# Optimization experiments

Hardware: AMD Instinct MI355X
Metric: run time of the kernel (lower is better)

## Reference

```python
import jax, jax.numpy as jnp
import numpy as np
import math

EMB = 2048
HEADS = 16
HEAD_DIM = EMB // HEADS  # 128
SCALE = math.sqrt(HEAD_DIM)


def srms_norm(x, eps_min=1e-12):
    # Scaled RMS norm over last dim, computed in float32.
    d = x.shape[-1]
    xf = x.astype(jnp.float32)
    norm = jnp.linalg.norm(xf * (1.0 / math.sqrt(d)), axis=-1, keepdims=True)
    norm = jnp.maximum(norm, eps_min)
    return (xf / norm).astype(x.dtype)


def setup_inputs() -> dict:
    key = jax.random.key(0)
    ks = jax.random.split(key, 6)
    x = jax.random.normal(ks[0], (4, 4096, EMB), dtype=jnp.float32)
    # xavier-normal std for square D x D: sqrt(2/(D+D)) = 1/sqrt(D); gain=1 (lth=None)
    std = 1.0 / math.sqrt(EMB)
    Wq = jax.random.normal(ks[1], (EMB, EMB), dtype=jnp.float32) * std
    Wk = jax.random.normal(ks[2], (EMB, EMB), dtype=jnp.float32) * std
    Wv = jax.random.normal(ks[3], (EMB, EMB), dtype=jnp.float32) * std
    Wu = jax.random.normal(ks[4], (EMB, EMB), dtype=jnp.float32) * std
    Wo = jax.random.normal(ks[5], (EMB, EMB), dtype=jnp.float32) * std
    return {"x": x, "Wq": Wq, "Wk": Wk, "Wv": Wv, "Wu": Wu, "Wo": Wo}


def reference(x, Wq, Wk, Wv, Wu, Wo):
    B, L, D = x.shape
    H, dh = HEADS, HEAD_DIM
    # projections (weights stored as [in, out])
    q = (x @ Wq).reshape(B, L, H, dh).transpose(0, 2, 1, 3)  # [B,H,L,dh]
    k = (x @ Wk).reshape(B, L, H, dh).transpose(0, 2, 1, 3)
    v = (x @ Wv).reshape(B, L, H, dh).transpose(0, 2, 1, 3)
    u = (x @ Wu).reshape(B, L, H, dh).transpose(0, 2, 1, 3)
    q = jax.nn.relu(q) / SCALE
    k = jax.nn.relu(k) / SCALE
    u = jax.nn.silu(u)
    # linear retention: kv state [B,H,dh,dh], then q @ kv
    kv = jnp.einsum('bhlk,bhlv->bhkv', k, v)
    out = jnp.einsum('bhlk,bhkv->bhlv', q, kv)
    out = srms_norm(out) * u
    out = out.transpose(0, 2, 1, 3).reshape(B, L, D)
    return out @ Wo
```

## Files before the change

### kernel.cpp

```cpp
#include <hip/hip_runtime.h>
#include <hip/hip_bf16.h>
#include <cstdint>


typedef __attribute__((ext_vector_type(8))) short short8;
typedef __attribute__((ext_vector_type(4))) float f32x4;

#define DEVI static __device__ __forceinline__

DEVI float bf2f(unsigned short u) {
    union { unsigned int i; float f; } w; w.i = ((unsigned int)u) << 16; return w.f;
}
DEVI unsigned short f2bf(float f) {
    union { float f; unsigned int i; } w; w.f = f;
    return (unsigned short)((w.i + 0x7fffu + ((w.i >> 16) & 1u)) >> 16);
}

#define GLDS16(gp, lp) __builtin_amdgcn_global_load_lds( \
    (const __attribute__((address_space(1))) void*)(gp), \
    (__attribute__((address_space(3))) void*)(lp), 16, 0, 0)

__global__ void probe_dtype(const unsigned short* __restrict__ x, int* flag) {
    __shared__ int cnt;
    if (threadIdx.x == 0) cnt = 0;
    __syncthreads();
    int c = 0;
    for (int i = threadIdx.x; i < 4096; i += 256) {
        float a = fabsf(bf2f(x[i]));
        if (!(a <= 1e4f) || (a != 0.0f && a < 1e-4f)) ++c;
    }
    atomicAdd(&cnt, c);
    __syncthreads();
    if (threadIdx.x == 0) *flag = (cnt < 512) ? 1 : 0;
}

__global__ void wconvert(const void* __restrict__ Wq, const void* __restrict__ Wk,
                         const void* __restrict__ Wv, const void* __restrict__ Wu,
                         const void* __restrict__ Wo,
                         unsigned short* __restrict__ wt4,
                         unsigned short* __restrict__ wot,
                         const int* __restrict__ flag) {
    const int z = blockIdx.z;
    const void* W = (z == 0) ? Wq : (z == 1) ? Wk : (z == 2) ? Wv : (z == 3) ? Wu : Wo;
    const bool isbf = (*flag != 0);
    __shared__ float tile[32][33];
    const int j0 = blockIdx.x * 32, i0 = blockIdx.y * 32;
    const int tx = threadIdx.x, ty = threadIdx.y;
#pragma unroll
    for (int r = 0; r < 4; ++r) {
        const int i = i0 + ty * 4 + r;
        float v;
        if (isbf) v = bf2f(((const unsigned short*)W)[i * 2048 + j0 + tx]);
        else      v = ((const float*)W)[i * 2048 + j0 + tx];
        tile[ty * 4 + r][tx] = v;
    }
    __syncthreads();
#pragma unroll
    for (int r = 0; r < 4; ++r) {
        const int j = j0 + ty * 4 + r;
        const unsigned short bv = f2bf(tile[tx][ty * 4 + r]);
        if (z < 4) wt4[(long)(z * 2048 + j) * 2048 + i0 + tx] = bv;
        else       wot[(long)j * 2048 + i0 + tx] = bv;
    }
}

__global__ void xconvert(const void* __restrict__ X, unsigned short* __restrict__ xb,
                         const int* __restrict__ flag) {
    const bool isbf = (*flag != 0);
    const long i = (long)blockIdx.x * 256 + threadIdx.x;
    if (isbf) {
        ((uint4*)xb)[i] = ((const uint4*)X)[i];
    } else {
        const float4 f0 = ((const float4*)X)[2 * i];
        const float4 f1 = ((const float4*)X)[2 * i + 1];
        union { unsigned short us[8]; uint4 v; } o;
        o.us[0] = f2bf(f0.x); o.us[1] = f2bf(f0.y); o.us[2] = f2bf(f0.z); o.us[3] = f2bf(f0.w);
        o.us[4] = f2bf(f1.x); o.us[5] = f2bf(f1.y); o.us[6] = f2bf(f1.z); o.us[7] = f2bf(f1.w);
        ((uint4*)xb)[i] = o.v;
    }
}

__global__ void gemm_qkvu(const unsigned short* __restrict__ Xb,
                          const unsigned short* __restrict__ Wt4,
                          unsigned short* __restrict__ Qb, unsigned short* __restrict__ Kb,
                          unsigned short* __restrict__ Vb, unsigned short* __restrict__ Ub) {
    __shared__ unsigned short As[128 * 32];
    __shared__ unsigned short Bs[128 * 32];
    const int orig = blockIdx.x;
    const int swz = (orig & 7) * 1024 + (orig >> 3);
    const int m0 = (swz & 127) * 128;
    const int nt = swz >> 7;
    const int j0 = nt * 128;
    const int tid = threadIdx.x;
    const int wave = tid >> 6, lane = tid & 63;
    const int wr = wave >> 1, wc = wave & 1;
    const int srow = tid >> 2;
    const int scol = (tid & 3) * 8;
    f32x4 acc[4][4] = {};

    for (int kt = 0; kt < 64; ++kt) {
        __syncthreads();
        const int kb = kt * 32;
#pragma unroll
        for (int i = 0; i < 2; ++i) {
            GLDS16(Xb  + (long)(m0 + i * 64 + srow) * 2048 + kb + scol, As + i * 2048 + wave * 512);
            GLDS16(Wt4 + (long)(j0 + i * 64 + srow) * 2048 + kb + scol, Bs + i * 2048 + wave * 512);
        }
        __syncthreads();
        short8 a[4], b[4];
#pragma unroll
        for (int fm = 0; fm < 4; ++fm)
            a[fm] = *(const short8*)(As + (wr * 64 + fm * 16 + (lane & 15)) * 32 + (lane >> 4) * 8);
#pragma unroll
        for (int fn = 0; fn < 4; ++fn)
            b[fn] = *(const short8*)(Bs + (wc * 64 + fn * 16 + (lane & 15)) * 32 + (lane >> 4) * 8);
#pragma unroll
        for (int fm = 0; fm < 4; ++fm)
#pragma unroll
            for (int fn = 0; fn < 4; ++fn)
                acc[fm][fn] = __builtin_amdgcn_mfma_f32_16x16x32_bf16(a[fm], b[fn], acc[fm][fn], 0, 0, 0);
    }

    const int seg = nt >> 4;
    unsigned short* outp = (seg == 0) ? Qb : (seg == 1) ? Kb : (seg == 2) ? Vb : Ub;
    const int cl0 = (nt & 15) * 128 + wc * 64;
#pragma unroll
    for (int fm = 0; fm < 4; ++fm) {
#pragma unroll
        for (int fn = 0; fn < 4; ++fn) {
            const int col = cl0 + fn * 16 + (lane & 15);
#pragma unroll
            for (int r = 0; r < 4; ++r) {
                const long row = m0 + wr * 64 + fm * 16 + ((lane >> 4) << 2) + r;
                float v = acc[fm][fn][r];
                if (seg <= 1)      v = fmaxf(v, 0.0f) * 0.08838834764831845f;
                else if (seg == 3) v = v / (1.0f + __expf(-v));
                outp[row * 2048 + col] = f2bf(v);
            }
        }
    }
}

__global__ void kv_accum(const unsigned short* __restrict__ Kb,
                         const unsigned short* __restrict__ Vb,
                         float* __restrict__ KVpart) {
    __shared__ unsigned short Kt[128 * 64];
    __shared__ unsigned short Vt[128 * 64];
    const int bh = blockIdx.x;
    const int chunk = blockIdx.y;
    const int b = bh >> 4, h = bh & 15;
    const int t = threadIdx.x, wave = t >> 6, lane = t & 63;
    const int wr = wave >> 1, wc = wave & 1;
    const int l0 = (t & 15) * 4;
    const int dkg = t >> 4;
    const long gbase = ((long)b * 4096 + chunk * 1024) * 2048 + h * 128;
    f32x4 acc[4][4] = {};

    for (int tile = 0; tile < 16; ++tile) {
        __syncthreads();
        short8 kr[4], vr[4];
#pragma unroll
        for (int li = 0; li < 4; ++li) {
            const long go = gbase + (long)(tile * 64 + l0 + li) * 2048 + dkg * 8;
            kr[li] = *(const short8*)(Kb + go);
            vr[li] = *(const short8*)(Vb + go);
        }
#pragma unroll
        for (int i = 0; i < 8; ++i) {
            const int row = dkg * 8 + i;
            const int lin = row * 128 + l0 * 2;
            const int off = (lin ^ ((row & 7) << 4)) >> 1;
            union { unsigned short us[4]; unsigned long long u; } pk, pv;
#pragma unroll
            for (int li = 0; li < 4; ++li) { pk.us[li] = (unsigned short)kr[li][i]; pv.us[li] = (unsigned short)vr[li][i]; }
            *(unsigned long long*)(Kt + off) = pk.u;
            *(unsigned long long*)(Vt + off) = pv.u;
        }
        __syncthreads();
#pragma unroll
        for (int ks = 0; ks < 2; ++ks) {
            const int kof = ks * 64 + (lane >> 4) * 16;
            short8 a[4], bfr[4];
#pragma unroll
            for (int f = 0; f < 4; ++f) {
                const int ra = wr * 64 + f * 16 + (lane & 15);
                const int rb = wc * 64 + f * 16 + (lane & 15);
                a[f]   = *(const short8*)(Vt + (((ra * 128 + kof) ^ ((ra & 7) << 4)) >> 1));
                bfr[f] = *(const short8*)(Kt + (((rb * 128 + kof) ^ ((rb & 7) << 4)) >> 1));
            }
#pragma unroll
            for (int fm = 0; fm < 4; ++fm)
#pragma unroll
                for (int fn = 0; fn < 4; ++fn)
                    acc[fm][fn] = __builtin_amdgcn_mfma_f32_16x16x32_bf16(a[fm], bfr[fn], acc[fm][fn], 0, 0, 0);
        }
    }
    float* dst = KVpart + ((long)chunk * 64 + bh) * 16384;
#pragma unroll
    for (int fm = 0; fm < 4; ++fm)
#pragma unroll
        for (int fn = 0; fn < 4; ++fn)
#pragma unroll
            for (int r = 0; r < 4; ++r) {
                const int dv = wr * 64 + fm * 16 + ((lane >> 4) << 2) + r;
                const int dk = wc * 64 + fn * 16 + (lane & 15);
                dst[dv * 128 + dk] = acc[fm][fn][r];
            }
}

__global__ void kv_finalize(const float* __restrict__ KVpart,
                            unsigned short* __restrict__ KVhi,
                            unsigned short* __restrict__ KVlo) {
    const long base = ((long)blockIdx.x * 256 + threadIdx.x) * 4;
    float4 s0 = *(const float4*)(KVpart + base);
    const float4 s1 = *(const float4*)(KVpart + 1048576 + base);
    const float4 s2 = *(const float4*)(KVpart + 2097152 + base);
    const float4 s3 = *(const float4*)(KVpart + 3145728 + base);
    float s[4] = { s0.x + s1.x + s2.x + s3.x, s0.y + s1.y + s2.y + s3.y,
                   s0.z + s1.z + s2.z + s3.z, s0.w + s1.w + s2.w + s3.w };
    union { unsigned short us[4]; unsigned long long u; } hi, lo;
#pragma unroll
    for (int j = 0; j < 4; ++j) {
        hi.us[j] = f2bf(s[j]);
        lo.us[j] = f2bf(s[j] - bf2f(hi.us[j]));
    }
    *(unsigned long long*)(KVhi + base) = hi.u;
    *(unsigned long long*)(KVlo + base) = lo.u;
}

__global__ void o_norm(const unsigned short* __restrict__ Qb,
                       const unsigned short* __restrict__ Ub,
                       const unsigned short* __restrict__ KVhi,
                       const unsigned short* __restrict__ KVlo,
                       unsigned short* __restrict__ Ob) {
    __shared__ unsigned short Qs[128 * 128];
    const int tid = threadIdx.x, wave = tid >> 6, lane = tid & 63;
    const int tile = blockIdx.x;
    const int bh = blockIdx.y;
    const int b = bh >> 4, h = bh & 15;
    const long n0 = (long)b * 4096 + tile * 128;

    const int qrow = tid >> 4;
    const int qcol = (tid & 15) * 8;
#pragma unroll
    for (int i = 0; i < 8; ++i)
        GLDS16(Qb + (n0 + i * 16 + qrow) * 2048 + h * 128 + qcol, Qs + i * 2048 + wave * 512);
    __syncthreads();

    const unsigned short* KH = KVhi + (long)bh * 16384;
    const unsigned short* KL = KVlo + (long)bh * 16384;
    f32x4 acc[2][8] = {};
#pragma unroll
    for (int kk = 0; kk < 4; ++kk) {
        const short8 a0 = *(const short8*)(Qs + (wave * 32 + (lane & 15)) * 128 + kk * 32 + (lane >> 4) * 8);
        const short8 a1 = *(const short8*)(Qs + (wave * 32 + 16 + (lane & 15)) * 128 + kk * 32 + (lane >> 4) * 8);
#pragma unroll
        for (int fn = 0; fn < 8; ++fn) {
            const int bo = (fn * 16 + (lane & 15)) * 128 + kk * 32 + (lane >> 4) * 8;
            const short8 bhi = *(const short8*)(KH + bo);
            const short8 blo = *(const short8*)(KL + bo);
            acc[0][fn] = __builtin_amdgcn_mfma_f32_16x16x32_bf16(a0, bhi, acc[0][fn], 0, 0, 0);
            acc[0][fn] = __builtin_amdgcn_mfma_f32_16x16x32_bf16(a0, blo, acc[0][fn], 0, 0, 0);
            acc[1][fn] = __builtin_amdgcn_mfma_f32_16x16x32_bf16(a1, bhi, acc[1][fn], 0, 0, 0);
            acc[1][fn] = __builtin_amdgcn_mfma_f32_16x16x32_bf16(a1, blo, acc[1][fn], 0, 0, 0);
        }
    }

#pragma unroll
    for (int fm = 0; fm < 2; ++fm) {
#pragma unroll
        for (int r = 0; r < 4; ++r) {
            float ssq = 0.0f;
#pragma unroll
            for (int fn = 0; fn < 8; ++fn) { const float v = acc[fm][fn][r]; ssq += v * v; }
            ssq += __shfl_xor(ssq, 1);
            ssq += __shfl_xor(ssq, 2);
            ssq += __shfl_xor(ssq, 4);
            ssq += __shfl_xor(ssq, 8);
            const float nrm = fmaxf(sqrtf(ssq) * 0.08838834764831845f, 1e-12f);
            const float scl = 1.0f / nrm;
            const long row = n0 + wave * 32 + fm * 16 + ((lane >> 4) << 2) + r;
#pragma unroll
            for (int fn = 0; fn < 8; ++fn) {
                const int col = fn * 16 + (lane & 15);
                const float uv = bf2f(Ub[row * 2048 + h * 128 + col]);
                Ob[row * 2048 + h * 128 + col] = f2bf(acc[fm][fn][r] * scl * uv);
            }
        }
    }
}

__global__ void gemm_out(const unsigned short* __restrict__ Obuf,
                         const unsigned short* __restrict__ Wot,
                         void* __restrict__ out, const int* __restrict__ flag) {
    __shared__ unsigned short As[128 * 32];
    __shared__ unsigned short Bs[128 * 32];
    const int orig = blockIdx.x;
    const int swz = (orig & 7) * 256 + (orig >> 3);
    const int m0 = (swz & 127) * 128;
    const int j0 = (swz >> 7) * 128;
    const int tid = threadIdx.x;
    const int wave = tid >> 6, lane = tid & 63;
    const int wr = wave >> 1, wc = wave & 1;
    const int srow = tid >> 2;
    const int scol = (tid & 3) * 8;
    f32x4 acc[4][4] = {};

    for (int kt = 0; kt < 64; ++kt) {
        __syncthreads();
        const int kb = kt * 32;
#pragma unroll
        for (int i = 0; i < 2; ++i) {
            GLDS16(Obuf + (long)(m0 + i * 64 + srow) * 2048 + kb + scol, As + i * 2048 + wave * 512);
            GLDS16(Wot  + (long)(j0 + i * 64 + srow) * 2048 + kb + scol, Bs + i * 2048 + wave * 512);
        }
        __syncthreads();
        short8 a[4], b[4];
#pragma unroll
        for (int fm = 0; fm < 4; ++fm)
            a[fm] = *(const short8*)(As + (wr * 64 + fm * 16 + (lane & 15)) * 32 + (lane >> 4) * 8);
#pragma unroll
        for (int fn = 0; fn < 4; ++fn)
            b[fn] = *(const short8*)(Bs + (wc * 64 + fn * 16 + (lane & 15)) * 32 + (lane >> 4) * 8);
#pragma unroll
        for (int fm = 0; fm < 4; ++fm)
#pragma unroll
            for (int fn = 0; fn < 4; ++fn)
                acc[fm][fn] = __builtin_amdgcn_mfma_f32_16x16x32_bf16(a[fm], b[fn], acc[fm][fn], 0, 0, 0);
    }

    const bool isbf = (*flag != 0);
#pragma unroll
    for (int fm = 0; fm < 4; ++fm) {
#pragma unroll
        for (int fn = 0; fn < 4; ++fn) {
            const int col = j0 + wc * 64 + fn * 16 + (lane & 15);
#pragma unroll
            for (int r = 0; r < 4; ++r) {
                const long row = m0 + wr * 64 + fm * 16 + ((lane >> 4) << 2) + r;
                const float v = acc[fm][fn][r];
                if (isbf) ((unsigned short*)out)[row * 2048 + col] = f2bf(v);
                else      ((float*)out)[row * 2048 + col] = v;
            }
        }
    }
}

extern "C" void kernel_launch(void* const* d_in, const int* in_sizes, int n_in,
                              void* d_out, int out_size, void* d_ws, size_t ws_size,
                              hipStream_t stream) {
    (void)in_sizes; (void)n_in; (void)out_size; (void)ws_size;
    char* ws = (char*)d_ws;
    unsigned short* Xb  = (unsigned short*)(ws + 0);
    unsigned short* Wt4 = (unsigned short*)(ws + 67108864);
    unsigned short* Wot = (unsigned short*)(ws + 100663296);
    unsigned short* Qb  = (unsigned short*)(ws + 109051904);
    unsigned short* Kb  = (unsigned short*)(ws + 176160768);
    unsigned short* Vb  = (unsigned short*)(ws + 243269632);
    unsigned short* Ub  = (unsigned short*)(ws + 310378496);
    int*            flag= (int*)(ws + 381681664);
    float*          KVpart = (float*)Wt4;
    unsigned short* KVhi   = (unsigned short*)(ws + 67108864 + 16777216);
    unsigned short* KVlo   = (unsigned short*)(ws + 67108864 + 18874368);
    unsigned short* Ob     = Xb;

    probe_dtype<<<1, 256, 0, stream>>>((const unsigned short*)d_in[0], flag);
    wconvert<<<dim3(64, 64, 5), dim3(32, 8), 0, stream>>>(d_in[1], d_in[2], d_in[3],
                                                          d_in[4], d_in[5], Wt4, Wot, flag);
    xconvert<<<16384, 256, 0, stream>>>(d_in[0], Xb, flag);
    gemm_qkvu<<<8192, 256, 0, stream>>>(Xb, Wt4, Qb, Kb, Vb, Ub);
    kv_accum<<<dim3(64, 4), 256, 0, stream>>>(Kb, Vb, KVpart);
    kv_finalize<<<1024, 256, 0, stream>>>(KVpart, KVhi, KVlo);
    o_norm<<<dim3(32, 64), 256, 0, stream>>>(Qb, Ub, KVhi, KVlo, Ob);
    gemm_out<<<2048, 256, 0, stream>>>(Ob, Wot, d_out, flag);
}
```

Measured before the change: 1.109 ms.

## Rewrite projection GEMMs with 256x256 tiles, 4-stage LDS pipeline and swizzle

Both the QKVU and output GEMMs now share a core that uses 256x256 block tiles with 8 waves and a 4-deep ring of LDS buffers. Global-to-LDS loads are issued three stages ahead, with vmcnt waits in place of full syncthreads, and reads use an XOR-swizzled LDS layout to avoid bank conflicts. The core also raises wave priority around the MFMA block. The aim is more reuse per tile and memory latency hidden behind MFMA work, at the cost of 128KB of LDS per block, higher register pressure, and fewer blocks in flight.

```diff
diff --git a/kernel.cpp b/kernel.cpp
--- a/kernel.cpp
+++ b/kernel.cpp
@@ -80,62 +80,126 @@
     }
 }
 
-__global__ void gemm_qkvu(const unsigned short* __restrict__ Xb,
-                          const unsigned short* __restrict__ Wt4,
-                          unsigned short* __restrict__ Qb, unsigned short* __restrict__ Kb,
-                          unsigned short* __restrict__ Vb, unsigned short* __restrict__ Ub) {
-    __shared__ unsigned short As[128 * 32];
-    __shared__ unsigned short Bs[128 * 32];
+DEVI void gemm_core(const unsigned short* __restrict__ Ag,
+                    const unsigned short* __restrict__ Bg,
+                    unsigned short* As, unsigned short* Bs,
+                    f32x4 acc[8][4], const int tid) {
+    const int wave = tid >> 6, lane = tid & 63;
+    const int wr = wave >> 2, wc = wave & 3;
+    const int srow = tid >> 2;
+    const int lsl = (tid & 3) ^ ((srow >> 1) & 3);
+    const unsigned short* ga0 = Ag + (long)srow * 2048 + lsl * 8;
+    const unsigned short* ga1 = ga0 + 128 * 2048;
+    const unsigned short* gb0 = Bg + (long)srow * 2048 + lsl * 8;
+    const unsigned short* gb1 = gb0 + 128 * 2048;
+    const int ldsb = wave * 512;
+
+    const int psl = ((lane >> 4) ^ (((lane & 15) >> 1) & 3)) * 8;
+    const int abase = (wr * 128 + (lane & 15)) * 32 + psl;
+    const int bbase = (wc * 64 + (lane & 15)) * 32 + psl;
+
+#define ISSUE(tt) do { \
+    const int _b = (tt) & 3; const int _ko = (tt) * 32; \
+    GLDS16(ga0 + _ko, As + _b * 8192 + ldsb); \
+    GLDS16(ga1 + _ko, As + _b * 8192 + 4096 + ldsb); \
+    GLDS16(gb0 + _ko, Bs + _b * 8192 + ldsb); \
+    GLDS16(gb1 + _ko, Bs + _b * 8192 + 4096 + ldsb); \
+} while (0)
+
+    ISSUE(0); ISSUE(1); ISSUE(2);
+    for (int t = 0; t < 64; ++t) {
+        asm volatile("s_waitcnt vmcnt(8)" ::: "memory");
+        asm volatile("s_barrier" ::: "memory");
+        int tt = t + 3; if (tt >= 64) tt -= 64;
+        ISSUE(tt);
+        const unsigned short* a_ = As + (t & 3) * 8192;
+        const unsigned short* b_ = Bs + (t & 3) * 8192;
+        short8 af[8], bf[4];
+#pragma unroll
+        for (int fm = 0; fm < 8; ++fm) af[fm] = *(const short8*)(a_ + abase + fm * 512);
+#pragma unroll
+        for (int fn = 0; fn < 4; ++fn) bf[fn] = *(const short8*)(b_ + bbase + fn * 512);
+        __builtin_amdgcn_s_setprio(1);
+#pragma unroll
+        for (int fm = 0; fm < 8; ++fm)
+#pragma unroll
+            for (int fn = 0; fn < 4; ++fn)
+                acc[fm][fn] = __builtin_amdgcn_mfma_f32_16x16x32_bf16(af[fm], bf[fn], acc[fm][fn], 0, 0, 0);
+        __builtin_amdgcn_s_setprio(0);
+        asm volatile("s_barrier" ::: "memory");
+    }
+    asm volatile("s_waitcnt vmcnt(0)" ::: "memory");
+#undef ISSUE
+}
+
+__global__ __launch_bounds__(512, 2)
+void gemm_qkvu(const unsigned short* __restrict__ Xb,
+               const unsigned short* __restrict__ Wt4,
+               unsigned short* __restrict__ Qb, unsigned short* __restrict__ Kb,
+               unsigned short* __restrict__ Vb, unsigned short* __restrict__ Ub) {
+    __shared__ unsigned short As[4 * 8192];
+    __shared__ unsigned short Bs[4 * 8192];
     const int orig = blockIdx.x;
-    const int swz = (orig & 7) * 1024 + (orig >> 3);
-    const int m0 = (swz & 127) * 128;
-    const int nt = swz >> 7;
-    const int j0 = nt * 128;
+    const int flat = (orig & 7) * 256 + (orig >> 3);
+    const int mt = flat & 63, nt = flat >> 6;
+    const long m0 = (long)mt * 256;
     const int tid = threadIdx.x;
+    f32x4 acc[8][4] = {};
+
+    gemm_core(Xb + m0 * 2048, Wt4 + (long)nt * 256 * 2048, As, Bs, acc, tid);
+
     const int wave = tid >> 6, lane = tid & 63;
-    const int wr = wave >> 1, wc = wave & 1;
-    const int srow = tid >> 2;
-    const int scol = (tid & 3) * 8;
-    f32x4 acc[4][4] = {};
-
-    for (int kt = 0; kt < 64; ++kt) {
-        __syncthreads();
-        const int kb = kt * 32;
-#pragma unroll
-        for (int i = 0; i < 2; ++i) {
-            GLDS16(Xb  + (long)(m0 + i * 64 + srow) * 2048 + kb + scol, As + i * 2048 + wave * 512);
-            GLDS16(Wt4 + (long)(j0 + i * 64 + srow) * 2048 + kb + scol, Bs + i * 2048 + wave * 512);
-        }
-        __syncthreads();
-        short8 a[4], b[4];
-#pragma unroll
-        for (int fm = 0; fm < 4; ++fm)
-            a[fm] = *(const short8*)(As + (wr * 64 + fm * 16 + (lane & 15)) * 32 + (lane >> 4) * 8);
-#pragma unroll
-        for (int fn = 0; fn < 4; ++fn)
-            b[fn] = *(const short8*)(Bs + (wc * 64 + fn * 16 + (lane & 15)) * 32 + (lane >> 4) * 8);
-#pragma unroll
-        for (int fm = 0; fm < 4; ++fm)
-#pragma unroll
-            for (int fn = 0; fn < 4; ++fn)
-                acc[fm][fn] = __builtin_amdgcn_mfma_f32_16x16x32_bf16(a[fm], b[fn], acc[fm][fn], 0, 0, 0);
-    }
-
-    const int seg = nt >> 4;
+    const int wr = wave >> 2, wc = wave & 3;
+    const int seg = nt >> 3;
     unsigned short* outp = (seg == 0) ? Qb : (seg == 1) ? Kb : (seg == 2) ? Vb : Ub;
-    const int cl0 = (nt & 15) * 128 + wc * 64;
-#pragma unroll
-    for (int fm = 0; fm < 4; ++fm) {
+    const int cl0 = (nt & 7) * 256 + wc * 64;
+#pragma unroll
+    for (int fm = 0; fm < 8; ++fm) {
 #pragma unroll
         for (int fn = 0; fn < 4; ++fn) {
             const int col = cl0 + fn * 16 + (lane & 15);
 #pragma unroll
             for (int r = 0; r < 4; ++r) {
-                const long row = m0 + wr * 64 + fm * 16 + ((lane >> 4) << 2) + r;
+                const long row = m0 + wr * 128 + fm * 16 + ((lane >> 4) << 2) + r;
                 float v = acc[fm][fn][r];
                 if (seg <= 1)      v = fmaxf(v, 0.0f) * 0.08838834764831845f;
                 else if (seg == 3) v = v / (1.0f + __expf(-v));
                 outp[row * 2048 + col] = f2bf(v);
+            }
+        }
+    }
+}
+
+__global__ __launch_bounds__(512, 2)
+void gemm_out(const unsigned short* __restrict__ Obuf,
+              const unsigned short* __restrict__ Wot,
+              void* __restrict__ out, const int* __restrict__ flag) {
+    __shared__ unsigned short As[4 * 8192];
+    __shared__ unsigned short Bs[4 * 8192];
+    const int orig = blockIdx.x;
+    const int flat = (orig & 7) * 64 + (orig >> 3);
+    const int mt = flat & 63, nt = flat >> 6;
+    const long m0 = (long)mt * 256;
+    const int j0 = nt * 256;
+    const int tid = threadIdx.x;
+    f32x4 acc[8][4] = {};
+
+    gemm_core(Obuf + m0 * 2048, Wot + (long)j0 * 2048, As, Bs, acc, tid);
+
+    const int wave = tid >> 6, lane = tid & 63;
+    const int wr = wave >> 2, wc = wave & 3;
+    const bool isbf = (*flag != 0);
+#pragma unroll
+    for (int fm = 0; fm < 8; ++fm) {
+#pragma unroll
+        for (int fn = 0; fn < 4; ++fn) {
+            const int col = j0 + wc * 64 + fn * 16 + (lane & 15);
+#pragma unroll
+            for (int r = 0; r < 4; ++r) {
+                const long row = m0 + wr * 128 + fm * 16 + ((lane >> 4) << 2) + r;
+                const float v = acc[fm][fn][r];
+                if (isbf) ((unsigned short*)out)[row * 2048 + col] = f2bf(v);
+                else      ((float*)out)[row * 2048 + col] = v;
             }
         }
     }
@@ -285,62 +349,6 @@
                 const int col = fn * 16 + (lane & 15);
                 const float uv = bf2f(Ub[row * 2048 + h * 128 + col]);
                 Ob[row * 2048 + h * 128 + col] = f2bf(acc[fm][fn][r] * scl * uv);
-            }
-        }
-    }
-}
-
-__global__ void gemm_out(const unsigned short* __restrict__ Obuf,
-                         const unsigned short* __restrict__ Wot,
-                         void* __restrict__ out, const int* __restrict__ flag) {
-    __shared__ unsigned short As[128 * 32];
-    __shared__ unsigned short Bs[128 * 32];
-    const int orig = blockIdx.x;
-    const int swz = (orig & 7) * 256 + (orig >> 3);
-    const int m0 = (swz & 127) * 128;
-    const int j0 = (swz >> 7) * 128;
-    const int tid = threadIdx.x;
-    const int wave = tid >> 6, lane = tid & 63;
-    const int wr = wave >> 1, wc = wave & 1;
-    const int srow = tid >> 2;
-    const int scol = (tid & 3) * 8;
-    f32x4 acc[4][4] = {};
-
-    for (int kt = 0; kt < 64; ++kt) {
-        __syncthreads();
-        const int kb = kt * 32;
-#pragma unroll
-        for (int i = 0; i < 2; ++i) {
-            GLDS16(Obuf + (long)(m0 + i * 64 + srow) * 2048 + kb + scol, As + i * 2048 + wave * 512);
-            GLDS16(Wot  + (long)(j0 + i * 64 + srow) * 2048 + kb + scol, Bs + i * 2048 + wave * 512);
-        }
-        __syncthreads();
-        short8 a[4], b[4];
-#pragma unroll
-        for (int fm = 0; fm < 4; ++fm)
-            a[fm] = *(const short8*)(As + (wr * 64 + fm * 16 + (lane & 15)) * 32 + (lane >> 4) * 8);
-#pragma unroll
-        for (int fn = 0; fn < 4; ++fn)
-            b[fn] = *(const short8*)(Bs + (wc * 64 + fn * 16 + (lane & 15)) * 32 + (lane >> 4) * 8);
-#pragma unroll
-        for (int fm = 0; fm < 4; ++fm)
-#pragma unroll
-            for (int fn = 0; fn < 4; ++fn)
-                acc[fm][fn] = __builtin_amdgcn_mfma_f32_16x16x32_bf16(a[fm], b[fn], acc[fm][fn], 0, 0, 0);
-    }
-
-    const bool isbf = (*flag != 0);
-#pragma unroll
-    for (int fm = 0; fm < 4; ++fm) {
-#pragma unroll
-        for (int fn = 0; fn < 4; ++fn) {
-            const int col = j0 + wc * 64 + fn * 16 + (lane & 15);
-#pragma unroll
-            for (int r = 0; r < 4; ++r) {
-                const long row = m0 + wr * 64 + fm * 16 + ((lane >> 4) << 2) + r;
-                const float v = acc[fm][fn][r];
-                if (isbf) ((unsigned short*)out)[row * 2048 + col] = f2bf(v);
-                else      ((float*)out)[row * 2048 + col] = v;
             }
         }
     }
@@ -368,9 +376,9 @@
     wconvert<<<dim3(64, 64, 5), dim3(32, 8), 0, stream>>>(d_in[1], d_in[2], d_in[3],
                                                           d_in[4], d_in[5], Wt4, Wot, flag);
     xconvert<<<16384, 256, 0, stream>>>(d_in[0], Xb, flag);
-    gemm_qkvu<<<8192, 256, 0, stream>>>(Xb, Wt4, Qb, Kb, Vb, Ub);
+    gemm_qkvu<<<2048, 512, 0, stream>>>(Xb, Wt4, Qb, Kb, Vb, Ub);
     kv_accum<<<dim3(64, 4), 256, 0, stream>>>(Kb, Vb, KVpart);
     kv_finalize<<<1024, 256, 0, stream>>>(KVpart, KVhi, KVlo);
     o_norm<<<dim3(32, 64), 256, 0, stream>>>(Qb, Ub, KVhi, KVlo, Ob);
-    gemm_out<<<2048, 256, 0, stream>>>(Ob, Wot, d_out, flag);
-}
+    gemm_out<<<512, 512, 0, stream>>>(Ob, Wot, d_out, flag);
+}
```

After: 1.195 ms. +7.8%, slower.
